# Optimization experiments

Hardware: AMD Instinct MI355X
Metric: run time of the kernel (lower is better)

## Reference

```python
import jax, jax.numpy as jnp
import numpy as np

B, S, E, H = 2, 2048, 1024, 16
D = E // H  # head_dim = 64


def _rope_angles(seq_len, d, dtype=jnp.float32):
    # standard RoPE frequencies: theta_i = 10000^{-2i/d}
    inv_freq = 1.0 / (10000.0 ** (jnp.arange(0, d, 2, dtype=dtype) / d))  # [d/2]
    pos = jnp.arange(seq_len, dtype=dtype)                                # [S]
    ang = pos[:, None] * inv_freq[None, :]                                # [S, d/2]
    ang = jnp.concatenate([ang, ang], axis=-1)                            # [S, d]
    return jnp.cos(ang), jnp.sin(ang)


def _rotate_half(t):
    t1, t2 = jnp.split(t, 2, axis=-1)
    return jnp.concatenate([-t2, t1], axis=-1)


def _apply_rope(t, cos, sin):
    # t: [B, H, S, D]; cos/sin: [S, D]
    return t * cos[None, None, :, :] + _rotate_half(t) * sin[None, None, :, :]


def setup_inputs() -> dict:
    key = jax.random.key(0)
    ks = jax.random.split(key, 6)
    x = jax.random.normal(ks[0], (B, S, E), dtype=jnp.float32)
    mask = jnp.tril(jnp.ones((S, S), dtype=bool))  # causal: True = attend
    scale = 1.0 / np.sqrt(E)
    Wq = jax.random.normal(ks[1], (E, E), dtype=jnp.float32) * scale
    Wk = jax.random.normal(ks[2], (E, E), dtype=jnp.float32) * scale
    Wv = jax.random.normal(ks[3], (E, E), dtype=jnp.float32) * scale
    Wo = jax.random.normal(ks[4], (E, E), dtype=jnp.float32) * scale
    z = jnp.zeros((E,), dtype=jnp.float32)
    return {"x": x, "mask": mask, "Wq": Wq, "bq": z, "Wk": Wk, "bk": z,
            "Wv": Wv, "bv": z, "Wo": Wo, "bo": z}


def reference(x, mask, Wq, bq, Wk, bk, Wv, bv, Wo, bo):
    b, s, e = x.shape
    # QKV projections (nn.Linear convention: y = x @ W.T + b)
    def proj(W, bias):
        y = jnp.einsum('bse,fe->bsf', x, W) + bias
        return y.reshape(b, s, H, D).transpose(0, 2, 1, 3)  # [B,H,S,D]
    q, k, v = proj(Wq, bq), proj(Wk, bk), proj(Wv, bv)
    # RoPE on q and k (per-head rotary over head_dim)
    cos, sin = _rope_angles(s, D, dtype=x.dtype)
    q = _apply_rope(q, cos, sin)
    k = _apply_rope(k, cos, sin)
    # SDPA with boolean mask (True = attend)
    scores = jnp.einsum('bhqd,bhkd->bhqk', q, k) / jnp.sqrt(jnp.asarray(D, x.dtype))
    neg = jnp.asarray(jnp.finfo(x.dtype).min, x.dtype)
    scores = jnp.where(mask[None, None, :, :], scores, neg)
    attn = jax.nn.softmax(scores, axis=-1)
    out = jnp.einsum('bhqk,bhkd->bhqd', attn, v)          # [B,H,S,D]
    out = out.transpose(0, 2, 1, 3).reshape(b, s, e)       # [B,S,E]
    return jnp.einsum('bse,fe->bsf', out, Wo) + bo
```

## Files before the change

kernel.cpp:

```cpp
#include <hip/hip_runtime.h>
#include <hip/hip_bf16.h>

typedef unsigned short u16;
typedef unsigned int u32;
typedef __bf16 bf16x8 __attribute__((ext_vector_type(8)));
typedef float f32x4 __attribute__((ext_vector_type(4)));

#define S_LEN 2048
#define NHEAD 16
#define HDIM  64
#define EMB   1024
#define BATCH 2

__device__ __forceinline__ float bf2f(u16 u) {
  union { unsigned int i; float f; } c; c.i = ((unsigned int)u) << 16; return c.f;
}
__device__ __forceinline__ u16 f2bf(float f) {
  union { float f; unsigned int i; } c; c.f = f;
  unsigned int i = c.i;
  return (u16)((i + 0x7FFFu + ((i >> 16) & 1u)) >> 16);
}
__device__ __forceinline__ u16 f2bf_trunc(float f) {
  union { float f; unsigned int i; } c; c.f = f;
  return (u16)(c.i >> 16);
}
__device__ __forceinline__ f32x4 mfma16(bf16x8 a, bf16x8 b, f32x4 c) {
  return __builtin_amdgcn_mfma_f32_16x16x32_bf16(a, b, c, 0, 0, 0);
}
__device__ __forceinline__ void cp16(const u16* g, u16* l) {
  __builtin_amdgcn_global_load_lds(
      (const __attribute__((address_space(1))) u32*)g,
      (__attribute__((address_space(3))) u32*)l, 16, 0, 0);
}

__global__ __launch_bounds__(256) void convert_kernel(
    const void* __restrict__ x, const void* __restrict__ Wq,
    const void* __restrict__ Wk, const void* __restrict__ Wv,
    const void* __restrict__ Wo,
    u16* __restrict__ xb, u16* __restrict__ wqb, u16* __restrict__ wkb,
    u16* __restrict__ wvb, u16* __restrict__ wob,
    int* __restrict__ flag, float2* __restrict__ tab)
{
  __shared__ int s_flag;
  if (threadIdx.x == 0) s_flag = 0;
  __syncthreads();
  {
    const u16* xs = (const u16*)x;
    u16 w0 = xs[threadIdx.x * 2], w1 = xs[threadIdx.x * 2 + 1];
    if ((((w0 >> 7) & 0xFF) >= 0xC0) || (((w1 >> 7) & 0xFF) >= 0xC0))
      atomicOr(&s_flag, 1);
  }
  __syncthreads();
  const int f32io = s_flag;
  if (blockIdx.x == 0 && threadIdx.x == 0) flag[0] = f32io;

  size_t gid = (size_t)blockIdx.x * 256 + threadIdx.x;
  size_t e = gid * 8;
  const void* src; u16* dst; size_t off;
  if (e < 4194304) { src = x; dst = xb; off = e; }
  else {
    size_t rr = e - 4194304;
    int j = (int)(rr >> 20); off = rr & 1048575;
    src = (j == 0) ? Wq : (j == 1) ? Wk : (j == 2) ? Wv : Wo;
    dst = (j == 0) ? wqb : (j == 1) ? wkb : (j == 2) ? wvb : wob;
  }
  if (f32io) {
    const float* s = (const float*)src + off;
    float4 a = *(const float4*)s;
    float4 b2 = *(const float4*)(s + 4);
    ushort4 u0; u0.x = f2bf(a.x); u0.y = f2bf(a.y); u0.z = f2bf(a.z); u0.w = f2bf(a.w);
    ushort4 u1; u1.x = f2bf(b2.x); u1.y = f2bf(b2.y); u1.z = f2bf(b2.z); u1.w = f2bf(b2.w);
    *(ushort4*)(dst + off) = u0;
    *(ushort4*)(dst + off + 4) = u1;
  } else {
    *(uint4*)(dst + off) = *(const uint4*)((const u16*)src + off);
  }

  if (blockIdx.x < 256) {
    int id = blockIdx.x * 256 + threadIdx.x;
    int s = id >> 5, i = id & 31;
    float f = exp2f(-(float)i * 0.41524101186092029f);
    float ang = (float)s * f;
    tab[id] = make_float2(cosf(ang), sinf(ang));
  }
}

__device__ __forceinline__ void gemm_core_db(
    const u16* __restrict__ A, const u16* __restrict__ W,
    int m0, int n0, int t, f32x4 (&acc)[4][4],
    u16* __restrict__ Ash, u16* __restrict__ Bsh)
{
  const int lane = t & 63, lr = lane & 15, quad = lane >> 4;
  const int wv = t >> 6;
  const int wm = (wv & 1) * 64, wn = (wv >> 1) * 64;
  const int r0 = t >> 2;
  const int r1 = (t + 256) >> 2;
  const int c0 = (((t & 3) ^ ((t >> 2) & 3))) * 8;
  const int lds0 = (t & 192) * 8;
  const int lds1 = (256 + (t & 192)) * 8;
  const int qx = ((quad ^ (lr & 3))) * 8;
  const u16* gA0 = A + (size_t)(m0 + r0) * 1024 + c0;
  const u16* gA1 = A + (size_t)(m0 + r1) * 1024 + c0;
  const u16* gB0 = W + (size_t)(n0 + r0) * 1024 + c0;
  const u16* gB1 = W + (size_t)(n0 + r1) * 1024 + c0;

  cp16(gA0, Ash + lds0); cp16(gA1, Ash + lds1);
  cp16(gB0, Bsh + lds0); cp16(gB1, Bsh + lds1);
  __syncthreads();

  for (int kt = 0; kt < 1024; kt += 32) {
    const int cur = (kt >> 5) & 1;
    const u16* Ac = Ash + cur * 4096;
    const u16* Bc = Bsh + cur * 4096;
    bf16x8 af[4], bfr[4];
#pragma unroll
    for (int mi = 0; mi < 4; ++mi)
      af[mi] = *(const bf16x8*)(Ac + (wm + mi * 16 + lr) * 32 + qx);
#pragma unroll
    for (int ni = 0; ni < 4; ++ni)
      bfr[ni] = *(const bf16x8*)(Bc + (wn + ni * 16 + lr) * 32 + qx);
    if (kt + 32 < 1024) {
      u16* An = Ash + (1 - cur) * 4096;
      u16* Bn = Bsh + (1 - cur) * 4096;
      cp16(gA0 + kt + 32, An + lds0); cp16(gA1 + kt + 32, An + lds1);
      cp16(gB0 + kt + 32, Bn + lds0); cp16(gB1 + kt + 32, Bn + lds1);
    }
#pragma unroll
    for (int mi = 0; mi < 4; ++mi)
#pragma unroll
      for (int ni = 0; ni < 4; ++ni)
        acc[mi][ni] = mfma16(af[mi], bfr[ni], acc[mi][ni]);
    __syncthreads();
  }
}

__device__ __forceinline__ void gemm_epilogue(
    int mode, int f32io, f32x4 (&acc)[4][4],
    const void* biasvp, void* outvp, int m0, int n0, int t,
    const float2* __restrict__ tab)
{
  const int lane = t & 63, lr = lane & 15, quad = lane >> 4;
  const int wv = t >> 6;
  const int wm = (wv & 1) * 64, wn = (wv >> 1) * 64;
  const float* biasf = (const float*)biasvp;
  const u16* biasb = (const u16*)biasvp;
#define BIASV(n) (f32io ? biasf[(n)] : bf2f(biasb[(n)]))
  if (mode == 1) {
    u16* Out = (u16*)outvp;
#pragma unroll
    for (int mi = 0; mi < 4; ++mi) {
#pragma unroll
      for (int r = 0; r < 4; ++r) {
        int mm = m0 + wm + mi * 16 + quad * 4 + r;
        int s = mm & (S_LEN - 1), b = mm >> 11;
        float2 cs0 = tab[s * 32 + lr];
        float2 cs1 = tab[s * 32 + 16 + lr];
#pragma unroll
        for (int ni = 0; ni < 4; ++ni) {
          int n = n0 + wn + ni * 16 + lr;
          int h = n >> 6, d = n & 63;
          float v  = acc[mi][ni][r]     + BIASV(n);
          float vp = acc[mi][ni ^ 2][r] + BIASV(n ^ 32);
          float rot = (d < 32) ? -vp : vp;
          float cc = (ni & 1) ? cs1.x : cs0.x;
          float ss = (ni & 1) ? cs1.y : cs0.y;
          size_t off = (((size_t)(b * NHEAD + h)) * S_LEN + s) * HDIM + d;
          Out[off] = f2bf(v * cc + rot * ss);
        }
      }
    }
  } else if (mode == 2) {
    u16* Out = (u16*)outvp;
#pragma unroll
    for (int mi = 0; mi < 4; ++mi) {
      int mm = m0 + wm + mi * 16 + quad * 4;
      int s = mm & (S_LEN - 1), b = mm >> 11;
#pragma unroll
      for (int ni = 0; ni < 4; ++ni) {
        int n = n0 + wn + ni * 16 + lr;
        int h = n >> 6, d = n & 63;
        float bv = BIASV(n);
        u16 p0 = f2bf(acc[mi][ni][0] + bv);
        u16 p1 = f2bf(acc[mi][ni][1] + bv);
        u16 p2 = f2bf(acc[mi][ni][2] + bv);
        u16 p3 = f2bf(acc[mi][ni][3] + bv);
        uint2 pk = make_uint2((u32)p0 | ((u32)p1 << 16),
                              (u32)p2 | ((u32)p3 << 16));
        size_t off = (((size_t)(b * NHEAD + h)) * HDIM + d) * S_LEN + s;
        *(uint2*)(Out + off) = pk;
      }
    }
  }
#undef BIASV
}

__global__ __launch_bounds__(256) void gemm_qkv(
    const u16* __restrict__ A, const u16* __restrict__ Wq,
    const u16* __restrict__ Wk, const u16* __restrict__ Wv,
    const void* bq, const void* bk, const void* bv,
    u16* qo, u16* ko, u16* vo, const int* __restrict__ dflag,
    const float2* __restrict__ tab)
{
  alignas(16) __shared__ u16 Ash[2 * 128 * 32];
  alignas(16) __shared__ u16 Bsh[2 * 128 * 32];
  const int lin = blockIdx.y * 24 + blockIdx.x;
  const int xcd = lin & 7, rr = lin >> 3;
  const int mt = (xcd << 2) + (rr & 3);
  const int nw = rr >> 2;
  const int wsel = nw >> 3;
  const u16* W = (wsel == 0) ? Wq : (wsel == 1) ? Wk : Wv;
  const void* bias = (wsel == 0) ? bq : (wsel == 1) ? bk : bv;
  void* out = (wsel == 0) ? (void*)qo : (wsel == 1) ? (void*)ko : (void*)vo;
  const int mode = (wsel == 2) ? 2 : 1;
  const int m0 = mt * 128, n0 = (nw & 7) * 128;
  f32x4 acc[4][4];
  const f32x4 zero4 = {0.f, 0.f, 0.f, 0.f};
#pragma unroll
  for (int i = 0; i < 4; ++i)
#pragma unroll
    for (int j = 0; j < 4; ++j) acc[i][j] = zero4;
  gemm_core_db(A, W, m0, n0, threadIdx.x, acc, Ash, Bsh);
  gemm_epilogue(mode, dflag[0], acc, bias, out, m0, n0, threadIdx.x, tab);
}

__global__ __launch_bounds__(256) void gemm_out(
    const u16* __restrict__ A, const u16* __restrict__ W,
    const void* bias, void* out, const int* __restrict__ dflag)
{
  alignas(16) __shared__ u16 Ash[2 * 64 * 32];
  alignas(16) __shared__ u16 Bsh[2 * 128 * 32];
  const int t = threadIdx.x, lane = t & 63, wv = t >> 6;
  const int lr = lane & 15, quad = lane >> 4;
  const int lin = blockIdx.y * 8 + blockIdx.x;
  const int xcd = lin & 7, rl = lin >> 3;
  const int mt = (xcd << 3) + (rl & 7);
  const int m0 = mt * 64, n0 = (rl >> 3) * 128;
  const int wm = (wv & 1) * 32, wn = (wv >> 1) * 64;
  const int f32io = dflag[0];

  const int r0 = t >> 2;
  const int r1 = (t + 256) >> 2;
  const int c0 = (((t & 3) ^ ((t >> 2) & 3))) * 8;
  const int lds0 = (t & 192) * 8;
  const int lds1 = (256 + (t & 192)) * 8;
  const int qx = ((quad ^ (lr & 3))) * 8;
  const u16* gA0 = A + (size_t)(m0 + (r0 & 63)) * 1024 + c0;
  const u16* gB0 = W + (size_t)(n0 + r0) * 1024 + c0;
  const u16* gB1 = W + (size_t)(n0 + r1) * 1024 + c0;

  f32x4 acc[2][4];
  const f32x4 zero4 = {0.f, 0.f, 0.f, 0.f};
#pragma unroll
  for (int i = 0; i < 2; ++i)
#pragma unroll
    for (int j = 0; j < 4; ++j) acc[i][j] = zero4;

  cp16(gA0, Ash + lds0);
  cp16(gB0, Bsh + lds0); cp16(gB1, Bsh + lds1);
  __syncthreads();

  for (int kt = 0; kt < 1024; kt += 32) {
    const int cur = (kt >> 5) & 1;
    const u16* Ac = Ash + cur * 2048;
    const u16* Bc = Bsh + cur * 4096;
    bf16x8 af[2], bfr[4];
#pragma unroll
    for (int mi = 0; mi < 2; ++mi)
      af[mi] = *(const bf16x8*)(Ac + (wm + mi * 16 + lr) * 32 + qx);
#pragma unroll
    for (int ni = 0; ni < 4; ++ni)
      bfr[ni] = *(const bf16x8*)(Bc + (wn + ni * 16 + lr) * 32 + qx);
    if (kt + 32 < 1024) {
      u16* An = Ash + (1 - cur) * 2048;
      u16* Bn = Bsh + (1 - cur) * 4096;
      cp16(gA0 + kt + 32, An + lds0);
      cp16(gB0 + kt + 32, Bn + lds0); cp16(gB1 + kt + 32, Bn + lds1);
    }
#pragma unroll
    for (int mi = 0; mi < 2; ++mi)
#pragma unroll
      for (int ni = 0; ni < 4; ++ni)
        acc[mi][ni] = mfma16(af[mi], bfr[ni], acc[mi][ni]);
    __syncthreads();
  }

  const float* biasf = (const float*)bias;
  const u16* biasb = (const u16*)bias;
  float* Outf = (float*)out;
  u16* Outb = (u16*)out;
#pragma unroll
  for (int mi = 0; mi < 2; ++mi) {
#pragma unroll
    for (int r = 0; r < 4; ++r) {
      int mm = m0 + wm + mi * 16 + quad * 4 + r;
#pragma unroll
      for (int ni = 0; ni < 4; ++ni) {
        int n = n0 + wn + ni * 16 + lr;
        float bv = f32io ? biasf[n] : bf2f(biasb[n]);
        float v = acc[mi][ni][r] + bv;
        size_t off = (size_t)mm * 1024 + n;
        if (f32io) Outf[off] = v; else Outb[off] = f2bf(v);
      }
    }
  }
}

__device__ __forceinline__ void attn_phase(
    const bf16x8 (&qf)[2], f32x4 (&oacc)[4], f32x4& ls4,
    const u16 (*__restrict__ Ksh)[72], const u16 (*__restrict__ Vsh)[72],
    u16 (*__restrict__ Pw)[72], const bf16x8 ones,
    int kv0, int q0w, bool diag, int lr, int quad)
{
  const f32x4 zero4 = {0.f, 0.f, 0.f, 0.f};
  f32x4 sc[4];
#pragma unroll
  for (int ni = 0; ni < 4; ++ni) {
    bf16x8 kf0 = *(const bf16x8*)&Ksh[ni * 16 + lr][quad * 8];
    bf16x8 kf1 = *(const bf16x8*)&Ksh[ni * 16 + lr][32 + quad * 8];
    f32x4 z = zero4;
    z = mfma16(kf0, qf[0], z);
    z = mfma16(kf1, qf[1], z);
    sc[ni] = z;
  }
  const int qa = q0w + lr;
  if (diag) {
#pragma unroll
    for (int ni = 0; ni < 4; ++ni)
#pragma unroll
      for (int r = 0; r < 4; ++r) {
        float sarg = sc[ni][r] * 0.18033688f - 21.64042561f;
        if (kv0 + ni * 16 + quad * 4 + r > qa) sarg = -1e4f;
        sc[ni][r] = exp2f(sarg);
      }
  } else {
#pragma unroll
    for (int ni = 0; ni < 4; ++ni)
#pragma unroll
      for (int r = 0; r < 4; ++r)
        sc[ni][r] = exp2f(sc[ni][r] * 0.18033688f - 21.64042561f);
  }
#pragma unroll
  for (int ni = 0; ni < 4; ++ni) {
    u32 lo = (u32)f2bf_trunc(sc[ni][0]) | ((u32)f2bf_trunc(sc[ni][1]) << 16);
    u32 hi = (u32)f2bf_trunc(sc[ni][2]) | ((u32)f2bf_trunc(sc[ni][3]) << 16);
    *(uint2*)&Pw[lr][ni * 16 + quad * 4] = make_uint2(lo, hi);
  }
  bf16x8 pa0 = *(const bf16x8*)&Pw[lr][quad * 8];
  bf16x8 pa1 = *(const bf16x8*)&Pw[lr][32 + quad * 8];
  ls4 = mfma16(pa0, ones, ls4);
  ls4 = mfma16(pa1, ones, ls4);
#pragma unroll
  for (int oni = 0; oni < 4; ++oni) {
    bf16x8 vf0 = *(const bf16x8*)&Vsh[oni * 16 + lr][quad * 8];
    bf16x8 vf1 = *(const bf16x8*)&Vsh[oni * 16 + lr][32 + quad * 8];
    oacc[oni] = mfma16(pa0, vf0, oacc[oni]);
    oacc[oni] = mfma16(pa1, vf1, oacc[oni]);
  }
}

__device__ __forceinline__ void attn_phase_half(
    const bf16x8 (&qf)[2], f32x4 (&oacc)[4], f32x4& ls4,
    const u16 (*__restrict__ Ksh)[72], const u16 (*__restrict__ Vsh)[72],
    u16 (*__restrict__ Pw)[72], const bf16x8 ones,
    int kv0, int q0w, bool diag, int half, int lr, int quad)
{
  const f32x4 zero4 = {0.f, 0.f, 0.f, 0.f};
  f32x4 sc[2];
#pragma unroll
  for (int i = 0; i < 2; ++i) {
    const int ni = half * 2 + i;
    bf16x8 kf0 = *(const bf16x8*)&Ksh[ni * 16 + lr][quad * 8];
    bf16x8 kf1 = *(const bf16x8*)&Ksh[ni * 16 + lr][32 + quad * 8];
    f32x4 z = zero4;
    z = mfma16(kf0, qf[0], z);
    z = mfma16(kf1, qf[1], z);
    sc[i] = z;
  }
  const int qa = q0w + lr;
  if (diag) {
#pragma unroll
    for (int i = 0; i < 2; ++i)
#pragma unroll
      for (int r = 0; r < 4; ++r) {
        float sarg = sc[i][r] * 0.18033688f - 21.64042561f;
        if (kv0 + (half * 2 + i) * 16 + quad * 4 + r > qa) sarg = -1e4f;
        sc[i][r] = exp2f(sarg);
      }
  } else {
#pragma unroll
    for (int i = 0; i < 2; ++i)
#pragma unroll
      for (int r = 0; r < 4; ++r)
        sc[i][r] = exp2f(sc[i][r] * 0.18033688f - 21.64042561f);
  }
#pragma unroll
  for (int i = 0; i < 2; ++i) {
    u32 lo = (u32)f2bf_trunc(sc[i][0]) | ((u32)f2bf_trunc(sc[i][1]) << 16);
    u32 hi = (u32)f2bf_trunc(sc[i][2]) | ((u32)f2bf_trunc(sc[i][3]) << 16);
    *(uint2*)&Pw[lr][(half * 2 + i) * 16 + quad * 4] = make_uint2(lo, hi);
  }
  bf16x8 pa = *(const bf16x8*)&Pw[lr][half * 32 + quad * 8];
  ls4 = mfma16(pa, ones, ls4);
#pragma unroll
  for (int oni = 0; oni < 4; ++oni) {
    bf16x8 vf = *(const bf16x8*)&Vsh[oni * 16 + lr][half * 32 + quad * 8];
    oacc[oni] = mfma16(pa, vf, oacc[oni]);
  }
}

__device__ __forceinline__ void attn_finish(
    f32x4 (&oacc)[4], const f32x4 ls4, u16* __restrict__ O,
    int bh, int q0w, int lr, int quad)
{
  const int b = bh >> 4, h = bh & 15;
#pragma unroll
  for (int r = 0; r < 4; ++r) {
    const float scale = 1.f / ls4[r];
#pragma unroll
    for (int oni = 0; oni < 4; ++oni) {
      int s = q0w + quad * 4 + r;
      int e = h * HDIM + oni * 16 + lr;
      O[((size_t)(b * S_LEN + s)) * EMB + e] = f2bf(oacc[oni][r] * scale);
    }
  }
}

__global__ __launch_bounds__(512, 4) void attn_kernel(
    const u16* __restrict__ Q, const u16* __restrict__ Kr,
    const u16* __restrict__ Vt, u16* __restrict__ O)
{
  alignas(16) __shared__ u16 SH[27648];
  u16 (*Kdb)[64][72] = reinterpret_cast<u16(*)[64][72]>(SH);
  u16 (*Vdb)[64][72] = reinterpret_cast<u16(*)[64][72]>(SH + 9216);
  u16 (*Psh)[16][72] = reinterpret_cast<u16(*)[16][72]>(SH + 18432);
  const int t = threadIdx.x, lane = t & 63, wv = t >> 6;
  const int lr = lane & 15, quad = lane >> 4;
  const int lin = blockIdx.y * 16 + blockIdx.x;
  const int xcd = lin & 7, rl = lin >> 3;
  const int bh = (xcd << 2) + (rl & 3);
  const int qtA = rl >> 2;
  const int qtB = 31 - qtA;
  const bool grpA = (wv < 4);
  const int q0own = (grpA ? qtA : qtB) * 64 + (wv & 3) * 16;
  const int q0B = qtB * 64 + (wv & 3) * 16;
  const size_t base = (size_t)bh * S_LEN * HDIM;

  bf16x8 ones;
  {
    union { u16 u[8]; bf16x8 v; } o;
#pragma unroll
    for (int i = 0; i < 8; ++i) o.u[i] = 0x3F80;
    ones = o.v;
  }

  bf16x8 qfO[2], qfH[2];
  {
    const u16* qrow = Q + base + (size_t)(q0own + lr) * HDIM + quad * 8;
    qfO[0] = *(const bf16x8*)qrow;
    qfO[1] = *(const bf16x8*)(qrow + 32);
  }
  if (grpA) {
    const u16* qrow = Q + base + (size_t)(q0B + lr) * HDIM + quad * 8;
    qfH[0] = *(const bf16x8*)qrow;
    qfH[1] = *(const bf16x8*)(qrow + 32);
  } else { qfH[0] = qfO[0]; qfH[1] = qfO[1]; }

  f32x4 oacc0[4], oacc1[4];
  const f32x4 zero4 = {0.f, 0.f, 0.f, 0.f};
  f32x4 ls0 = zero4, ls1 = zero4;
#pragma unroll
  for (int i = 0; i < 4; ++i) { oacc0[i] = zero4; oacc1[i] = zero4; }

  const int rr = t >> 3, cc = (t & 7) * 8;
  uint4 krg = *(const uint4*)(Kr + base + (size_t)rr * HDIM + cc);
  uint4 vrg = *(const uint4*)(Vt + base + (size_t)rr * S_LEN + cc);

  for (int j = 0; j <= qtB; ++j) {
    const int cur = j & 1;
    *(uint4*)&Kdb[cur][rr][cc] = krg;
    *(uint4*)&Vdb[cur][rr][cc] = vrg;
    __syncthreads();
    if (j < qtB) {
      const int kv1 = (j + 1) * 64;
      krg = *(const uint4*)(Kr + base + (size_t)(kv1 + rr) * HDIM + cc);
      vrg = *(const uint4*)(Vt + base + (size_t)rr * S_LEN + kv1 + cc);
    }
    if (j <= qtA) {
      attn_phase(qfO, oacc0, ls0, Kdb[cur], Vdb[cur], Psh[wv], ones,
                 j * 64, q0own, grpA && (j == qtA), lr, quad);
    } else if (grpA) {
      attn_phase_half(qfH, oacc1, ls1, Kdb[cur], Vdb[cur], Psh[wv], ones,
                      j * 64, q0B, j == qtB, 1, lr, quad);
    } else {
      attn_phase_half(qfO, oacc0, ls0, Kdb[cur], Vdb[cur], Psh[wv], ones,
                      j * 64, q0B, j == qtB, 0, lr, quad);
    }
  }

  __syncthreads();
  float* scm = (float*)&SH[0];
  if (grpA) {
    float* dst = scm + (size_t)(wv * 64 + lane) * 21;
#pragma unroll
    for (int oni = 0; oni < 4; ++oni)
#pragma unroll
      for (int r = 0; r < 4; ++r) dst[oni * 4 + r] = oacc1[oni][r];
#pragma unroll
    for (int r = 0; r < 4; ++r) dst[16 + r] = ls1[r];
  }
  __syncthreads();
  if (!grpA) {
    const float* src = scm + (size_t)((wv - 4) * 64 + lane) * 21;
#pragma unroll
    for (int oni = 0; oni < 4; ++oni)
#pragma unroll
      for (int r = 0; r < 4; ++r) oacc0[oni][r] += src[oni * 4 + r];
#pragma unroll
    for (int r = 0; r < 4; ++r) ls0[r] += src[16 + r];
  }
  attn_finish(oacc0, ls0, O, bh, q0own, lr, quad);
}

extern "C" void kernel_launch(void* const* d_in, const int* in_sizes, int n_in,
                              void* d_out, int out_size, void* d_ws, size_t ws_size,
                              hipStream_t stream) {
  const void* x  = d_in[0];
  const void* Wq = d_in[2]; const void* bq = d_in[3];
  const void* Wk = d_in[4]; const void* bk = d_in[5];
  const void* Wv = d_in[6]; const void* bv = d_in[7];
  const void* Wo = d_in[8]; const void* bo = d_in[9];

  char* ws = (char*)d_ws;
  int* flag = (int*)ws;
  u16* xb  = (u16*)(ws + 256);
  u16* qws = xb  + 4194304;
  u16* kws = qws + 4194304;
  u16* vws = kws + 4194304;
  u16* wqb = vws + 4194304;
  u16* wkb = wqb + 1048576;
  u16* wvb = wkb + 1048576;
  u16* wob = wvb + 1048576;
  float2* tab = (float2*)(wob + 1048576);
  u16* ows = xb;

  convert_kernel<<<4096, 256, 0, stream>>>(x, Wq, Wk, Wv, Wo,
                                           xb, wqb, wkb, wvb, wob, flag, tab);
  gemm_qkv<<<dim3(24, 32), 256, 0, stream>>>(xb, wqb, wkb, wvb,
                                             bq, bk, bv, qws, kws, vws, flag, tab);
  attn_kernel<<<dim3(16, 32), 512, 0, stream>>>(qws, kws, vws, ows);
  gemm_out<<<dim3(8, 64), 256, 0, stream>>>(ows, wob, bo, d_out, flag);
}
```

Before: 201.9 us.

## Restructure QKV and output GEMM main loops with explicit vmcnt-based prefetch pipelining

Rewrites the K-loop of both projection GEMMs as a manually unrolled two-stage pipeline. Each step issues the global-to-LDS copies for the tile two steps ahead, then waits with explicit s_waitcnt vmcnt counts and raw s_barrier instead of __syncthreads. The goal is to keep one tile of loads in flight across the MFMA work and avoid the full memory drains that __syncthreads forces. The price is hand-managed wait counts and barriers, which are fragile and would race if the counts are wrong.

```diff
diff --git a/kernel.cpp b/kernel.cpp
--- a/kernel.cpp
+++ b/kernel.cpp
@@ -32,6 +32,10 @@
       (const __attribute__((address_space(1))) u32*)g,
       (__attribute__((address_space(3))) u32*)l, 16, 0, 0);
 }
+#define LGKM0() asm volatile("s_waitcnt lgkmcnt(0)" ::: "memory")
+#define WAITVC(n) asm volatile("s_waitcnt vmcnt(" #n ")" ::: "memory")
+#define SBAR() do { __builtin_amdgcn_s_barrier(); \
+                    __builtin_amdgcn_sched_barrier(0); } while (0)
 
 __global__ __launch_bounds__(256) void convert_kernel(
     const void* __restrict__ x, const void* __restrict__ Wq,
@@ -85,7 +89,28 @@
   }
 }
 
-__device__ __forceinline__ void gemm_core_db(
+__device__ __forceinline__ void frags128(
+    const u16* __restrict__ Ac, const u16* __restrict__ Bc,
+    int wm, int wn, int lr, int qx, bf16x8 (&af)[4], bf16x8 (&bfr)[4])
+{
+#pragma unroll
+  for (int mi = 0; mi < 4; ++mi)
+    af[mi] = *(const bf16x8*)(Ac + (wm + mi * 16 + lr) * 32 + qx);
+#pragma unroll
+  for (int ni = 0; ni < 4; ++ni)
+    bfr[ni] = *(const bf16x8*)(Bc + (wn + ni * 16 + lr) * 32 + qx);
+}
+__device__ __forceinline__ void mfma44(
+    const bf16x8 (&af)[4], const bf16x8 (&bfr)[4], f32x4 (&acc)[4][4])
+{
+#pragma unroll
+  for (int mi = 0; mi < 4; ++mi)
+#pragma unroll
+    for (int ni = 0; ni < 4; ++ni)
+      acc[mi][ni] = mfma16(af[mi], bfr[ni], acc[mi][ni]);
+}
+
+__device__ __forceinline__ void gemm_core_dp(
     const u16* __restrict__ A, const u16* __restrict__ W,
     int m0, int n0, int t, f32x4 (&acc)[4][4],
     u16* __restrict__ Ash, u16* __restrict__ Bsh)
@@ -103,35 +128,37 @@
   const u16* gA1 = A + (size_t)(m0 + r1) * 1024 + c0;
   const u16* gB0 = W + (size_t)(n0 + r0) * 1024 + c0;
   const u16* gB1 = W + (size_t)(n0 + r1) * 1024 + c0;
-
-  cp16(gA0, Ash + lds0); cp16(gA1, Ash + lds1);
-  cp16(gB0, Bsh + lds0); cp16(gB1, Bsh + lds1);
-  __syncthreads();
-
-  for (int kt = 0; kt < 1024; kt += 32) {
-    const int cur = (kt >> 5) & 1;
-    const u16* Ac = Ash + cur * 4096;
-    const u16* Bc = Bsh + cur * 4096;
-    bf16x8 af[4], bfr[4];
-#pragma unroll
-    for (int mi = 0; mi < 4; ++mi)
-      af[mi] = *(const bf16x8*)(Ac + (wm + mi * 16 + lr) * 32 + qx);
-#pragma unroll
-    for (int ni = 0; ni < 4; ++ni)
-      bfr[ni] = *(const bf16x8*)(Bc + (wn + ni * 16 + lr) * 32 + qx);
-    if (kt + 32 < 1024) {
-      u16* An = Ash + (1 - cur) * 4096;
-      u16* Bn = Bsh + (1 - cur) * 4096;
-      cp16(gA0 + kt + 32, An + lds0); cp16(gA1 + kt + 32, An + lds1);
-      cp16(gB0 + kt + 32, Bn + lds0); cp16(gB1 + kt + 32, Bn + lds1);
-    }
-#pragma unroll
-    for (int mi = 0; mi < 4; ++mi)
-#pragma unroll
-      for (int ni = 0; ni < 4; ++ni)
-        acc[mi][ni] = mfma16(af[mi], bfr[ni], acc[mi][ni]);
-    __syncthreads();
-  }
+  u16* A0 = Ash;            u16* B0 = Bsh;
+  u16* A1 = Ash + 4096;     u16* B1 = Bsh + 4096;
+
+#define STAGE4(kt, Ad, Bd) do { \
+    cp16(gA0 + (kt), (Ad) + lds0); cp16(gA1 + (kt), (Ad) + lds1); \
+    cp16(gB0 + (kt), (Bd) + lds0); cp16(gB1 + (kt), (Bd) + lds1); } while (0)
+
+  STAGE4(0, A0, B0);
+  STAGE4(32, A1, B1);
+  WAITVC(4);
+  SBAR();
+
+  bf16x8 af[4], bfr[4];
+  for (int kt = 0; kt < 960; kt += 64) {
+    frags128(A0, B0, wm, wn, lr, qx, af, bfr);
+    LGKM0(); SBAR();
+    STAGE4(kt + 64, A0, B0);
+    mfma44(af, bfr, acc);
+    WAITVC(4); SBAR();
+    frags128(A1, B1, wm, wn, lr, qx, af, bfr);
+    LGKM0(); SBAR();
+    STAGE4(kt + 96, A1, B1);
+    mfma44(af, bfr, acc);
+    WAITVC(4); SBAR();
+  }
+  frags128(A0, B0, wm, wn, lr, qx, af, bfr);
+  mfma44(af, bfr, acc);
+  WAITVC(0); SBAR();
+  frags128(A1, B1, wm, wn, lr, qx, af, bfr);
+  mfma44(af, bfr, acc);
+#undef STAGE4
 }
 
 __device__ __forceinline__ void gemm_epilogue(
@@ -219,7 +246,7 @@
   for (int i = 0; i < 4; ++i)
 #pragma unroll
     for (int j = 0; j < 4; ++j) acc[i][j] = zero4;
-  gemm_core_db(A, W, m0, n0, threadIdx.x, acc, Ash, Bsh);
+  gemm_core_dp(A, W, m0, n0, threadIdx.x, acc, Ash, Bsh);
   gemm_epilogue(mode, dflag[0], acc, bias, out, m0, n0, threadIdx.x, tab);
 }
 
@@ -236,7 +263,6 @@
   const int mt = (xcd << 3) + (rl & 7);
   const int m0 = mt * 64, n0 = (rl >> 3) * 128;
   const int wm = (wv & 1) * 32, wn = (wv >> 1) * 64;
-  const int f32io = dflag[0];
 
   const int r0 = t >> 2;
   const int r1 = (t + 256) >> 2;
@@ -247,6 +273,8 @@
   const u16* gA0 = A + (size_t)(m0 + (r0 & 63)) * 1024 + c0;
   const u16* gB0 = W + (size_t)(n0 + r0) * 1024 + c0;
   const u16* gB1 = W + (size_t)(n0 + r1) * 1024 + c0;
+  u16* A0 = Ash;          u16* B0 = Bsh;
+  u16* A1 = Ash + 2048;   u16* B1 = Bsh + 4096;
 
   f32x4 acc[2][4];
   const f32x4 zero4 = {0.f, 0.f, 0.f, 0.f};
@@ -255,35 +283,51 @@
 #pragma unroll
     for (int j = 0; j < 4; ++j) acc[i][j] = zero4;
 
-  cp16(gA0, Ash + lds0);
-  cp16(gB0, Bsh + lds0); cp16(gB1, Bsh + lds1);
-  __syncthreads();
-
-  for (int kt = 0; kt < 1024; kt += 32) {
-    const int cur = (kt >> 5) & 1;
-    const u16* Ac = Ash + cur * 2048;
-    const u16* Bc = Bsh + cur * 4096;
-    bf16x8 af[2], bfr[4];
-#pragma unroll
-    for (int mi = 0; mi < 2; ++mi)
-      af[mi] = *(const bf16x8*)(Ac + (wm + mi * 16 + lr) * 32 + qx);
-#pragma unroll
-    for (int ni = 0; ni < 4; ++ni)
-      bfr[ni] = *(const bf16x8*)(Bc + (wn + ni * 16 + lr) * 32 + qx);
-    if (kt + 32 < 1024) {
-      u16* An = Ash + (1 - cur) * 2048;
-      u16* Bn = Bsh + (1 - cur) * 4096;
-      cp16(gA0 + kt + 32, An + lds0);
-      cp16(gB0 + kt + 32, Bn + lds0); cp16(gB1 + kt + 32, Bn + lds1);
-    }
-#pragma unroll
-    for (int mi = 0; mi < 2; ++mi)
-#pragma unroll
-      for (int ni = 0; ni < 4; ++ni)
-        acc[mi][ni] = mfma16(af[mi], bfr[ni], acc[mi][ni]);
-    __syncthreads();
-  }
-
+#define STAGE3(kt, Ad, Bd) do { \
+    cp16(gA0 + (kt), (Ad) + lds0); \
+    cp16(gB0 + (kt), (Bd) + lds0); cp16(gB1 + (kt), (Bd) + lds1); } while (0)
+#define FRAGS2(Ac, Bc) do { \
+_Pragma("unroll") \
+    for (int mi = 0; mi < 2; ++mi) \
+      af[mi] = *(const bf16x8*)((Ac) + (wm + mi * 16 + lr) * 32 + qx); \
+_Pragma("unroll") \
+    for (int ni = 0; ni < 4; ++ni) \
+      bfr[ni] = *(const bf16x8*)((Bc) + (wn + ni * 16 + lr) * 32 + qx); } while (0)
+#define MFMA24() do { \
+_Pragma("unroll") \
+    for (int mi = 0; mi < 2; ++mi) \
+_Pragma("unroll") \
+      for (int ni = 0; ni < 4; ++ni) \
+        acc[mi][ni] = mfma16(af[mi], bfr[ni], acc[mi][ni]); } while (0)
+
+  STAGE3(0, A0, B0);
+  STAGE3(32, A1, B1);
+  WAITVC(3);
+  SBAR();
+
+  bf16x8 af[2], bfr[4];
+  for (int kt = 0; kt < 960; kt += 64) {
+    FRAGS2(A0, B0);
+    LGKM0(); SBAR();
+    STAGE3(kt + 64, A0, B0);
+    MFMA24();
+    WAITVC(3); SBAR();
+    FRAGS2(A1, B1);
+    LGKM0(); SBAR();
+    STAGE3(kt + 96, A1, B1);
+    MFMA24();
+    WAITVC(3); SBAR();
+  }
+  FRAGS2(A0, B0);
+  MFMA24();
+  WAITVC(0); SBAR();
+  FRAGS2(A1, B1);
+  MFMA24();
+#undef STAGE3
+#undef FRAGS2
+#undef MFMA24
+
+  const int f32io = dflag[0];
   const float* biasf = (const float*)bias;
   const u16* biasb = (const u16*)bias;
   float* Outf = (float*)out;
```

Result: no change. 202.9 us (+0.5%).

## Load attention K/V tiles with async global-to-LDS copies into XOR-swizzled buffers

Applied to the files above, without the earlier changes.

The attention kernel now stages K and V tiles with direct global-to-shared async copies (cp16) instead of loading them into registers and storing to LDS. The padded 72-wide rows are replaced by unpadded 64-wide rows with an XOR swizzle on the 16-byte chunk index to avoid bank conflicts. This is meant to cut register pressure and the VGPR round trip in the K/V pipeline, and it shrinks LDS use. The cost is a dependence on cp16 completion semantics: the only wait is the barrier, so if cp16 needs an explicit vmcnt wait there is a race risk.

```diff
diff --git a/kernel.cpp b/kernel.cpp
--- a/kernel.cpp
+++ b/kernel.cpp
@@ -307,16 +307,17 @@
 
 __device__ __forceinline__ void attn_phase(
     const bf16x8 (&qf)[2], f32x4 (&oacc)[4], f32x4& ls4,
-    const u16 (*__restrict__ Ksh)[72], const u16 (*__restrict__ Vsh)[72],
+    const u16* __restrict__ Kc, const u16* __restrict__ Vc,
     u16 (*__restrict__ Pw)[72], const bf16x8 ones,
-    int kv0, int q0w, bool diag, int lr, int quad)
+    int kv0, int q0w, bool diag, int lr, int quad, int ck0, int ck1)
 {
   const f32x4 zero4 = {0.f, 0.f, 0.f, 0.f};
   f32x4 sc[4];
 #pragma unroll
   for (int ni = 0; ni < 4; ++ni) {
-    bf16x8 kf0 = *(const bf16x8*)&Ksh[ni * 16 + lr][quad * 8];
-    bf16x8 kf1 = *(const bf16x8*)&Ksh[ni * 16 + lr][32 + quad * 8];
+    const u16* krow = Kc + (ni * 16 + lr) * 64;
+    bf16x8 kf0 = *(const bf16x8*)(krow + ck0);
+    bf16x8 kf1 = *(const bf16x8*)(krow + ck1);
     f32x4 z = zero4;
     z = mfma16(kf0, qf[0], z);
     z = mfma16(kf1, qf[1], z);
@@ -351,8 +352,9 @@
   ls4 = mfma16(pa1, ones, ls4);
 #pragma unroll
   for (int oni = 0; oni < 4; ++oni) {
-    bf16x8 vf0 = *(const bf16x8*)&Vsh[oni * 16 + lr][quad * 8];
-    bf16x8 vf1 = *(const bf16x8*)&Vsh[oni * 16 + lr][32 + quad * 8];
+    const u16* vrow = Vc + (oni * 16 + lr) * 64;
+    bf16x8 vf0 = *(const bf16x8*)(vrow + ck0);
+    bf16x8 vf1 = *(const bf16x8*)(vrow + ck1);
     oacc[oni] = mfma16(pa0, vf0, oacc[oni]);
     oacc[oni] = mfma16(pa1, vf1, oacc[oni]);
   }
@@ -360,17 +362,19 @@
 
 __device__ __forceinline__ void attn_phase_half(
     const bf16x8 (&qf)[2], f32x4 (&oacc)[4], f32x4& ls4,
-    const u16 (*__restrict__ Ksh)[72], const u16 (*__restrict__ Vsh)[72],
+    const u16* __restrict__ Kc, const u16* __restrict__ Vc,
     u16 (*__restrict__ Pw)[72], const bf16x8 ones,
-    int kv0, int q0w, bool diag, int half, int lr, int quad)
+    int kv0, int q0w, bool diag, int half, int lr, int quad,
+    int ck0, int ck1)
 {
   const f32x4 zero4 = {0.f, 0.f, 0.f, 0.f};
   f32x4 sc[2];
 #pragma unroll
   for (int i = 0; i < 2; ++i) {
     const int ni = half * 2 + i;
-    bf16x8 kf0 = *(const bf16x8*)&Ksh[ni * 16 + lr][quad * 8];
-    bf16x8 kf1 = *(const bf16x8*)&Ksh[ni * 16 + lr][32 + quad * 8];
+    const u16* krow = Kc + (ni * 16 + lr) * 64;
+    bf16x8 kf0 = *(const bf16x8*)(krow + ck0);
+    bf16x8 kf1 = *(const bf16x8*)(krow + ck1);
     f32x4 z = zero4;
     z = mfma16(kf0, qf[0], z);
     z = mfma16(kf1, qf[1], z);
@@ -401,9 +405,10 @@
   }
   bf16x8 pa = *(const bf16x8*)&Pw[lr][half * 32 + quad * 8];
   ls4 = mfma16(pa, ones, ls4);
+  const int ckh = ((half * 4 + quad) ^ (lr & 7)) * 8;
 #pragma unroll
   for (int oni = 0; oni < 4; ++oni) {
-    bf16x8 vf = *(const bf16x8*)&Vsh[oni * 16 + lr][half * 32 + quad * 8];
+    bf16x8 vf = *(const bf16x8*)(Vc + (oni * 16 + lr) * 64 + ckh);
     oacc[oni] = mfma16(pa, vf, oacc[oni]);
   }
 }
@@ -429,10 +434,10 @@
     const u16* __restrict__ Q, const u16* __restrict__ Kr,
     const u16* __restrict__ Vt, u16* __restrict__ O)
 {
-  alignas(16) __shared__ u16 SH[27648];
-  u16 (*Kdb)[64][72] = reinterpret_cast<u16(*)[64][72]>(SH);
-  u16 (*Vdb)[64][72] = reinterpret_cast<u16(*)[64][72]>(SH + 9216);
-  u16 (*Psh)[16][72] = reinterpret_cast<u16(*)[16][72]>(SH + 18432);
+  alignas(16) __shared__ u16 SH[25600];
+  u16* Kbuf = SH;
+  u16* Vbuf = SH + 8192;
+  u16 (*Psh)[16][72] = reinterpret_cast<u16(*)[16][72]>(SH + 16384);
   const int t = threadIdx.x, lane = t & 63, wv = t >> 6;
   const int lr = lane & 15, quad = lane >> 4;
   const int lin = blockIdx.y * 16 + blockIdx.x;
@@ -444,6 +449,13 @@
   const int q0own = (grpA ? qtA : qtB) * 64 + (wv & 3) * 16;
   const int q0B = qtB * 64 + (wv & 3) * 16;
   const size_t base = (size_t)bh * S_LEN * HDIM;
+  const int ck0 = ((quad ^ (lr & 7))) * 8;
+  const int ck1 = (((quad + 4) ^ (lr & 7))) * 8;
+
+  const int sr = t >> 3, sc = (t & 7) ^ (sr & 7);
+  const int wub = (t & 448) * 8;
+  const u16* gK = Kr + base + (size_t)sr * HDIM + sc * 8;
+  const u16* gV = Vt + base + (size_t)sr * S_LEN + sc * 8;
 
   bf16x8 ones;
   {
@@ -471,29 +483,28 @@
 #pragma unroll
   for (int i = 0; i < 4; ++i) { oacc0[i] = zero4; oacc1[i] = zero4; }
 
-  const int rr = t >> 3, cc = (t & 7) * 8;
-  uint4 krg = *(const uint4*)(Kr + base + (size_t)rr * HDIM + cc);
-  uint4 vrg = *(const uint4*)(Vt + base + (size_t)rr * S_LEN + cc);
+  cp16(gK, Kbuf + wub);
+  cp16(gV, Vbuf + wub);
 
   for (int j = 0; j <= qtB; ++j) {
     const int cur = j & 1;
-    *(uint4*)&Kdb[cur][rr][cc] = krg;
-    *(uint4*)&Vdb[cur][rr][cc] = vrg;
     __syncthreads();
     if (j < qtB) {
       const int kv1 = (j + 1) * 64;
-      krg = *(const uint4*)(Kr + base + (size_t)(kv1 + rr) * HDIM + cc);
-      vrg = *(const uint4*)(Vt + base + (size_t)rr * S_LEN + kv1 + cc);
-    }
+      cp16(gK + (size_t)kv1 * HDIM, Kbuf + (cur ^ 1) * 4096 + wub);
+      cp16(gV + kv1,                Vbuf + (cur ^ 1) * 4096 + wub);
+    }
+    const u16* Kc = Kbuf + cur * 4096;
+    const u16* Vc = Vbuf + cur * 4096;
     if (j <= qtA) {
-      attn_phase(qfO, oacc0, ls0, Kdb[cur], Vdb[cur], Psh[wv], ones,
-                 j * 64, q0own, grpA && (j == qtA), lr, quad);
+      attn_phase(qfO, oacc0, ls0, Kc, Vc, Psh[wv], ones,
+                 j * 64, q0own, grpA && (j == qtA), lr, quad, ck0, ck1);
     } else if (grpA) {
-      attn_phase_half(qfH, oacc1, ls1, Kdb[cur], Vdb[cur], Psh[wv], ones,
-                      j * 64, q0B, j == qtB, 1, lr, quad);
+      attn_phase_half(qfH, oacc1, ls1, Kc, Vc, Psh[wv], ones,
+                      j * 64, q0B, j == qtB, 1, lr, quad, ck0, ck1);
     } else {
-      attn_phase_half(qfO, oacc0, ls0, Kdb[cur], Vdb[cur], Psh[wv], ones,
-                      j * 64, q0B, j == qtB, 0, lr, quad);
+      attn_phase_half(qfO, oacc0, ls0, Kc, Vc, Psh[wv], ones,
+                      j * 64, q0B, j == qtB, 0, lr, quad, ck0, ck1);
     }
   }
 
```

Measured after the change: 199.2 us. About the same (-1.3%).
